# Kernel optimization log

Hardware: AMD Instinct MI355X
Metric: run time of the kernel (lower is better)

The kernel has to match this reference:

```python
import jax, jax.numpy as jnp
import numpy as np

ORDER = 63
CODEBOOK_SIZE = 256
MIN_DATA = 1
N_ITER = 5
EPS = 1e-05
PERTURB = 1e-05


def setup_inputs() -> dict:
    key = jax.random.key(0)
    x = jax.random.normal(key, (131072, ORDER + 1), dtype=jnp.float32)
    return {"x": x}


def _e_step(x, cb, T):
    # squared euclidean distances via gram trick: (T, curr)
    d2 = jnp.sum(x * x, 1)[:, None] - 2.0 * (x @ cb.T) + jnp.sum(cb * cb, 1)[None, :]
    idx = jnp.argmin(d2, axis=1)
    xq = cb[idx]
    dist = jnp.sum((x - xq) ** 2) / T
    return idx, dist


def _m_step(x, idx, curr, key):
    D = x.shape[1]
    ones = jnp.ones((x.shape[0],), x.dtype)
    n_data = jax.ops.segment_sum(ones, idx, num_segments=curr)        # histc
    mask = n_data >= MIN_DATA
    sums = jax.ops.segment_sum(x, idx, num_segments=curr)             # scatter_add
    cent = sums / jnp.maximum(n_data, 1.0)[:, None]
    m = jnp.argmax(n_data)
    r = jax.random.normal(key, (curr, D), x.dtype) * PERTURB
    nm = (~mask).astype(x.dtype)
    # empty clusters reseeded from the largest cluster, perturbed
    new = jnp.where(mask[:, None], cent, cent[m][None, :] - r)
    cnt = jnp.sum(nm)
    corr = jnp.sum(r * nm[:, None], axis=0) / jnp.maximum(cnt, 1.0)
    new = new.at[m].add(jnp.where(cnt > 0, corr, jnp.zeros_like(corr)))
    return new


def _lbg(x):
    T, D = x.shape
    K = CODEBOOK_SIZE
    codebook = jnp.full((K, D), 1e10, x.dtype).at[0].set(jnp.mean(x, axis=0))
    distance = jnp.asarray(jnp.inf, x.dtype)
    base = jax.random.key(42)
    curr = 1
    split = 0
    while curr * 2 <= K:  # static loop over log2(K) binary splits
        key_s = jax.random.fold_in(base, split)
        kr, kloop = jax.random.split(key_s)
        r = jax.random.normal(kr, (curr, D), x.dtype) * PERTURB
        codebook = codebook.at[curr:2 * curr].set(codebook[:curr] - r).at[:curr].add(r)
        curr *= 2
        prev = distance

        def body(carry, n, curr=curr):
            cb, prev_d, dist, done, key = carry
            idx, d_new = _e_step(x, cb, T)
            change = jnp.abs(prev_d - d_new)
            conv = (n > 0) & (change / (d_new + 1e-16) < EPS)
            key, sub = jax.random.split(key)
            cb_new = _m_step(x, idx, curr, sub)
            stop = done | conv
            cb_out = jnp.where(stop, cb, cb_new)        # skip m-step on convergence/break
            dist_out = jnp.where(done, dist, d_new)     # distance assigned before break
            prev_out = jnp.where(stop, prev_d, d_new)
            return (cb_out, prev_out, dist_out, stop, key), None

        carry0 = (codebook[:curr], prev, distance, jnp.asarray(False), kloop)
        (cb_fin, _, distance, _, _), _ = jax.lax.scan(body, carry0, jnp.arange(N_ITER))
        codebook = codebook.at[:curr].set(cb_fin)
        split += 1
    return codebook, distance


def reference(x):
    return _lbg(x)
```

## Files before the change

### kernel.cpp

```cpp
#include <hip/hip_runtime.h>
#include <stdint.h>


#define NPTS 131072
#define DIMS 64
#define KCB  256

struct LbgState { float dist; float prev; unsigned int done; unsigned int k0, k1; unsigned int pad; };

__device__ __forceinline__ uint32_t rotl32(uint32_t v, int n){ return (v<<n)|(v>>(32-n)); }

__device__ __forceinline__ void tf2x32(uint32_t k0, uint32_t k1, uint32_t x0, uint32_t x1,
                                       uint32_t& o0, uint32_t& o1){
  uint32_t ks2 = k0 ^ k1 ^ 0x1BD11BDAu;
  x0 += k0; x1 += k1;
  #define TFR(r) { x0 += x1; x1 = rotl32(x1, r); x1 ^= x0; }
  TFR(13) TFR(15) TFR(26) TFR(6)
  x0 += k1; x1 += ks2 + 1u;
  TFR(17) TFR(29) TFR(16) TFR(24)
  x0 += ks2; x1 += k0 + 2u;
  TFR(13) TFR(15) TFR(26) TFR(6)
  x0 += k0; x1 += k1 + 3u;
  TFR(17) TFR(29) TFR(16) TFR(24)
  x0 += k1; x1 += ks2 + 4u;
  TFR(13) TFR(15) TFR(26) TFR(6)
  x0 += ks2; x1 += k0 + 5u;
  #undef TFR
  o0 = x0; o1 = x1;
}

__device__ __forceinline__ float xla_erfinv_f32(float x){
  float w = -log1pf(-x*x);
  float p;
  if (w < 5.0f){
    w = w - 2.5f;
    p = 2.81022636e-08f;
    p = fmaf(p, w, 3.43273939e-07f);
    p = fmaf(p, w, -3.5233877e-06f);
    p = fmaf(p, w, -4.39150654e-06f);
    p = fmaf(p, w, 0.00021858087f);
    p = fmaf(p, w, -0.00125372503f);
    p = fmaf(p, w, -0.00417768164f);
    p = fmaf(p, w, 0.246640727f);
    p = fmaf(p, w, 1.50140941f);
  } else {
    w = sqrtf(w) - 3.0f;
    p = -0.000200214257f;
    p = fmaf(p, w, 0.000100950558f);
    p = fmaf(p, w, 0.00134934322f);
    p = fmaf(p, w, -0.00367342844f);
    p = fmaf(p, w, 0.00573950773f);
    p = fmaf(p, w, -0.0076224613f);
    p = fmaf(p, w, 0.00943887047f);
    p = fmaf(p, w, 1.00167406f);
    p = fmaf(p, w, 2.83297682f);
  }
  return p * x;
}

__device__ __forceinline__ float jax_normal_elem(uint32_t k0, uint32_t k1, uint32_t j){
  uint32_t o0, o1; tf2x32(k0, k1, 0u, j, o0, o1);
  uint32_t bits = o0 ^ o1;
  uint32_t fb = (bits >> 9) | 0x3f800000u;
  float f = __uint_as_float(fb) - 1.0f;
  const float lo = -0.99999994f;
  float u = f * 2.0f + lo;
  u = fmaxf(lo, u);
  return 1.41421356f * xla_erfinv_f32(u);
}

__device__ void do_split(float* __restrict__ cb, float* __restrict__ cnorm,
                         unsigned long long* __restrict__ sums,
                         unsigned int* __restrict__ ndata,
                         unsigned long long* __restrict__ distacc,
                         LbgState* __restrict__ st, int curr, int split, int t){
  __shared__ uint32_t kr0s, kr1s;
  if (t == 0){
    uint32_t ks0, ks1, a0, a1, b0, b1;
    tf2x32(0u, 42u, 0u, (uint32_t)split, ks0, ks1);
    tf2x32(ks0, ks1, 0u, 0u, a0, a1);
    tf2x32(ks0, ks1, 0u, 1u, b0, b1);
    kr0s = a0; kr1s = a1;
    st->k0 = b0; st->k1 = b1;
    st->prev = st->dist;
    st->done = 0u;
  }
  __syncthreads();
  const int n = curr * DIMS;
  for (int e = t; e < n; e += 256){
    int c = e >> 6, d = e & 63;
    float rv = jax_normal_elem(kr0s, kr1s, (uint32_t)e) * 1e-5f;
    float old = cb[c*DIMS + d];
    cb[(curr + c)*DIMS + d] = old - rv;
    cb[c*DIMS + d]          = old + rv;
  }
  __syncthreads();
  const int c2 = curr * 2;
  for (int c = t; c < c2; c += 256){
    float s = 0.f;
    for (int d = 0; d < DIMS; d++){ float vv = cb[c*DIMS+d]; s += vv*vv; }
    cnorm[c] = s;
  }
  for (int e = t; e < c2*DIMS; e += 256) sums[e] = 0ull;
  for (int c = t; c < c2; c += 256) ndata[c] = 0u;
  if (t == 0) *distacc = 0ull;
}

__global__ void mean_kernel(const float* __restrict__ x, unsigned long long* __restrict__ macc,
                            float* __restrict__ cb, float* __restrict__ cnorm,
                            unsigned long long* __restrict__ sums,
                            unsigned int* __restrict__ ndata,
                            unsigned long long* __restrict__ distacc,
                            LbgState* __restrict__ st, unsigned int* __restrict__ mcnt){
  __shared__ double part[256];
  __shared__ float stage[16*64];
  __shared__ int islast;
  const int t = threadIdx.x;
  const int d = t & 63;
  const int w = t >> 6;
  const size_t base = (size_t)blockIdx.x * 1024;
  const int lrow = t >> 4;
  const int lcol = (t & 15) * 4;

  const float4* xg = reinterpret_cast<const float4*>(x);
  float4 nxt = xg[((base + lrow) * DIMS + lcol) >> 2];
  double s = 0.0;
  for (int tt = 0; tt < 64; tt++){
    float4 cur = nxt;
    if (tt < 63)
      nxt = xg[((base + (tt+1)*16 + lrow) * DIMS + lcol) >> 2];
    __syncthreads();
    *reinterpret_cast<float4*>(&stage[lrow*DIMS + lcol]) = cur;
    __syncthreads();
    s += (double)stage[(w    )*DIMS + d];
    s += (double)stage[(w + 4)*DIMS + d];
    s += (double)stage[(w + 8)*DIMS + d];
    s += (double)stage[(w +12)*DIMS + d];
  }
  part[t] = s;
  __syncthreads();
  if (t < 64){
    double tot = part[t] + part[64+t] + part[128+t] + part[192+t];
    atomicAdd(&macc[t], (unsigned long long)__double2ll_rn(tot * 1099511627776.0));
  }
  __threadfence();
  __syncthreads();
  if (t == 0) islast = (atomicAdd(mcnt, 1u) == (unsigned)(gridDim.x - 1));
  __syncthreads();
  if (!islast) return;

  if (t < 64){
    long long mv = (long long)atomicAdd(&macc[t], 0ull);
    double mean = (double)mv * (1.0/1099511627776.0) / 131072.0;
    cb[t] = (float)mean;
  }
  for (int e = t; e < KCB*DIMS; e += 256)
    if (e >= 64) cb[e] = 1e10f;
  if (t == 0){
    st->dist = __builtin_inff();
    st->prev = __builtin_inff();
    st->done = 0u;
    atomicExch(mcnt, 0u);
  }
  __syncthreads();
  do_split(cb, cnorm, sums, ndata, distacc, st, 1, 0, t);
}

template<int CURR>
__global__ __launch_bounds__(256, 4)
void estep_kernel(const float* __restrict__ x, const float* __restrict__ cb,
                  const float* __restrict__ cnorm, unsigned char* __restrict__ bidx8,
                  unsigned long long* __restrict__ distacc, const LbgState* __restrict__ st){
  if (st->done) return;
  const int t = threadIdx.x;
  const int lane = t & 63;
  const int p = blockIdx.x * 256 + t;

  float xv[DIMS];
  const float4* xp = reinterpret_cast<const float4*>(x + (size_t)p * DIMS);
  #pragma unroll
  for (int i = 0; i < 16; i++){
    float4 v = xp[i];
    xv[4*i+0] = v.x; xv[4*i+1] = v.y; xv[4*i+2] = v.z; xv[4*i+3] = v.w;
  }
  float xx = 0.f;
  #pragma unroll
  for (int d = 0; d < DIMS; d++) xx += xv[d] * xv[d];

  constexpr int NJ = (CURR < 4) ? CURR : 4;
  float best = __builtin_inff();
  int bi = 0;
  for (int j0 = 0; j0 < CURR; j0 += NJ){
    const float* crow = cb + (size_t)j0 * DIMS;
    float acc[NJ];
    #pragma unroll
    for (int k = 0; k < NJ; k++) acc[k] = 0.f;
    #pragma unroll
    for (int d = 0; d < DIMS; d++){
      #pragma unroll
      for (int k = 0; k < NJ; k++)
        acc[k] = fmaf(xv[d], crow[k*DIMS + d], acc[k]);
    }
    #pragma unroll
    for (int k = 0; k < NJ; k++){
      float d2 = (xx - 2.0f*acc[k]) + cnorm[j0 + k];
      if (d2 < best){ best = d2; bi = j0 + k; }
    }
  }
  bidx8[p] = (unsigned char)bi;

  double dd = 0.0;
  const float4* cbv = reinterpret_cast<const float4*>(cb + (size_t)bi * DIMS);
  #pragma unroll
  for (int i = 0; i < 16; i++){
    float4 b = cbv[i];
    float df, sq;
    df = xv[4*i+0] - b.x; sq = df*df; dd += (double)sq;
    df = xv[4*i+1] - b.y; sq = df*df; dd += (double)sq;
    df = xv[4*i+2] - b.z; sq = df*df; dd += (double)sq;
    df = xv[4*i+3] - b.w; sq = df*df; dd += (double)sq;
  }
  for (int off = 32; off > 0; off >>= 1) dd += __shfl_down(dd, off);
  if (lane == 0)
    atomicAdd(distacc, (unsigned long long)__double2ll_rn(dd * 4294967296.0));
}

template<int CURR>
__global__ __launch_bounds__(256, 4)
void estep_sw(const float* __restrict__ x, const float* __restrict__ cb,
              const float* __restrict__ cnorm, unsigned char* __restrict__ bidx8,
              unsigned long long* __restrict__ distacc, const LbgState* __restrict__ st){
  if (st->done) return;
  constexpr int CPW = CURR / 4;
  constexpr int NJG = (CPW < 16) ? CPW : 16;
  constexpr int NG = CPW / NJG;
  __shared__ float4 xs[16*128];
  __shared__ float sxx[128];
  __shared__ float sbest[4*128];
  __shared__ int   sidx [4*128];
  __shared__ unsigned char sbidx[128];
  const int t = threadIdx.x;
  const int lane = t & 63;
  const int w = __builtin_amdgcn_readfirstlane(t >> 6);
  const int pbase = blockIdx.x * 128;

  {
    const int p = t & 127, h = t >> 7;
    const float4* xg = reinterpret_cast<const float4*>(x) + (size_t)(pbase + p) * 16 + h * 8;
    #pragma unroll
    for (int j = 0; j < 8; j++)
      xs[(h*8 + j)*128 + p] = xg[j];
  }
  __syncthreads();
  if (t < 128){
    float xx = 0.f;
    #pragma unroll
    for (int k4 = 0; k4 < 16; k4++){
      float4 v = xs[k4*128 + t];
      xx = fmaf(v.x, v.x, xx); xx = fmaf(v.y, v.y, xx);
      xx = fmaf(v.z, v.z, xx); xx = fmaf(v.w, v.w, xx);
    }
    sxx[t] = xx;
  }
  __syncthreads();

  const float xx0 = sxx[lane];
  const float xx1 = sxx[64 + lane];
  float best0 = __builtin_inff(), best1 = __builtin_inff();
  int bi0 = 0, bi1 = 0;
  const float4* cbg = reinterpret_cast<const float4*>(cb);
  const int cwbase = w * CPW;

  for (int g = 0; g < NG; g++){
    const int c0 = cwbase + g*NJG;
    float acc0[NJG], acc1[NJG];
    #pragma unroll
    for (int cj = 0; cj < NJG; cj++){ acc0[cj] = 0.f; acc1[cj] = 0.f; }
    for (int k4 = 0; k4 < 16; k4++){
      float4 xf0 = xs[k4*128 + lane];
      float4 xf1 = xs[k4*128 + 64 + lane];
      #pragma unroll
      for (int cj = 0; cj < NJG; cj++){
        float4 cf = cbg[(size_t)(c0 + cj)*16 + k4];
        acc0[cj] = fmaf(xf0.x, cf.x, acc0[cj]);
        acc0[cj] = fmaf(xf0.y, cf.y, acc0[cj]);
        acc0[cj] = fmaf(xf0.z, cf.z, acc0[cj]);
        acc0[cj] = fmaf(xf0.w, cf.w, acc0[cj]);
        acc1[cj] = fmaf(xf1.x, cf.x, acc1[cj]);
        acc1[cj] = fmaf(xf1.y, cf.y, acc1[cj]);
        acc1[cj] = fmaf(xf1.z, cf.z, acc1[cj]);
        acc1[cj] = fmaf(xf1.w, cf.w, acc1[cj]);
      }
    }
    #pragma unroll
    for (int cj = 0; cj < NJG; cj++){
      float cn = cnorm[c0 + cj];
      float d20 = (xx0 - 2.0f*acc0[cj]) + cn;
      if (d20 < best0){ best0 = d20; bi0 = c0 + cj; }
      float d21 = (xx1 - 2.0f*acc1[cj]) + cn;
      if (d21 < best1){ best1 = d21; bi1 = c0 + cj; }
    }
  }
  sbest[w*128 + lane]      = best0;  sidx[w*128 + lane]      = bi0;
  sbest[w*128 + 64 + lane] = best1;  sidx[w*128 + 64 + lane] = bi1;
  __syncthreads();

  if (t < 128){
    float best = sbest[t];
    int bi = sidx[t];
    #pragma unroll
    for (int ww = 1; ww < 4; ww++){
      float ob = sbest[ww*128 + t];
      int   oi = sidx [ww*128 + t];
      if (ob < best){ best = ob; bi = oi; }
    }
    sbidx[t] = (unsigned char)bi;
    bidx8[pbase + t] = (unsigned char)bi;
    const float4* cbv = cbg + (size_t)bi * 16;
    double dd = 0.0;
    #pragma unroll
    for (int k4 = 0; k4 < 16; k4++){
      float4 xv = xs[k4*128 + t];
      float4 b = cbv[k4];
      float df, sq;
      df = xv.x - b.x; sq = df*df; dd += (double)sq;
      df = xv.y - b.y; sq = df*df; dd += (double)sq;
      df = xv.z - b.z; sq = df*df; dd += (double)sq;
      df = xv.w - b.w; sq = df*df; dd += (double)sq;
    }
    for (int off = 32; off > 0; off >>= 1) dd += __shfl_down(dd, off);
    if ((t & 63) == 0)
      atomicAdd(distacc, (unsigned long long)__double2ll_rn(dd * 4294967296.0));
  }
}

template<int CURR, int NBLK>
__global__ __launch_bounds__(256)
void gather_kernel(const float* __restrict__ x, const unsigned char* __restrict__ bidx8,
                   unsigned long long* __restrict__ sums, unsigned int* __restrict__ ndata,
                   const LbgState* __restrict__ st){
  if (st->done) return;
  constexpr int CLOG = __builtin_ctz(CURR);
  constexpr int NCHUNK = NBLK / CURR;
  constexpr int PPC = NPTS / NCHUNK;
  constexpr int NPW = PPC / 4;
  __shared__ long long sacc[4*64];
  __shared__ unsigned int scw[4];
  const int t = threadIdx.x;
  const int lane = t & 63;
  const int w = t >> 6;
  const int c = blockIdx.x & (CURR - 1);
  const int chunk = blockIdx.x >> CLOG;
  const int pbase = chunk * PPC + w * NPW;

  long long acc = 0;
  unsigned int cnt = 0;
  int q0=0,q1=0,q2=0,q3=0,q4=0,q5=0,q6=0,q7=0, qn=0;
  const uint32_t* bp = reinterpret_cast<const uint32_t*>(bidx8 + pbase);
  for (int i = 0; i < NPW; i += 256){
    const uint32_t b4 = bp[(i >> 2) + lane];
    #pragma unroll
    for (int s = 0; s < 4; s++){
      unsigned long long m = __ballot(((b4 >> (8*s)) & 255u) == (unsigned)c);
      cnt += (unsigned int)__popcll(m);
      while (m){
        const int bit = __builtin_ctzll(m);
        m &= m - 1ull;
        const int p = pbase + i + bit*4 + s;
        if      (qn == 0) q0 = p;
        else if (qn == 1) q1 = p;
        else if (qn == 2) q2 = p;
        else if (qn == 3) q3 = p;
        else if (qn == 4) q4 = p;
        else if (qn == 5) q5 = p;
        else if (qn == 6) q6 = p;
        else              q7 = p;
        qn++;
        if (qn == 8){
          const float v0 = x[(size_t)q0 * DIMS + lane];
          const float v1 = x[(size_t)q1 * DIMS + lane];
          const float v2 = x[(size_t)q2 * DIMS + lane];
          const float v3 = x[(size_t)q3 * DIMS + lane];
          const float v4 = x[(size_t)q4 * DIMS + lane];
          const float v5 = x[(size_t)q5 * DIMS + lane];
          const float v6 = x[(size_t)q6 * DIMS + lane];
          const float v7 = x[(size_t)q7 * DIMS + lane];
          acc += (long long)__double2int_rn((double)v0 * 1048576.0);
          acc += (long long)__double2int_rn((double)v1 * 1048576.0);
          acc += (long long)__double2int_rn((double)v2 * 1048576.0);
          acc += (long long)__double2int_rn((double)v3 * 1048576.0);
          acc += (long long)__double2int_rn((double)v4 * 1048576.0);
          acc += (long long)__double2int_rn((double)v5 * 1048576.0);
          acc += (long long)__double2int_rn((double)v6 * 1048576.0);
          acc += (long long)__double2int_rn((double)v7 * 1048576.0);
          qn = 0;
        }
      }
    }
  }
  if (qn > 0){
    const int i1 = (qn > 1) ? q1 : q0;
    const int i2 = (qn > 2) ? q2 : q0;
    const int i3 = (qn > 3) ? q3 : q0;
    const int i4 = (qn > 4) ? q4 : q0;
    const int i5 = (qn > 5) ? q5 : q0;
    const int i6 = (qn > 6) ? q6 : q0;
    const float v0 = x[(size_t)q0 * DIMS + lane];
    const float v1 = x[(size_t)i1 * DIMS + lane];
    const float v2 = x[(size_t)i2 * DIMS + lane];
    const float v3 = x[(size_t)i3 * DIMS + lane];
    const float v4 = x[(size_t)i4 * DIMS + lane];
    const float v5 = x[(size_t)i5 * DIMS + lane];
    const float v6 = x[(size_t)i6 * DIMS + lane];
    acc += (long long)__double2int_rn((double)v0 * 1048576.0);
    if (qn > 1) acc += (long long)__double2int_rn((double)v1 * 1048576.0);
    if (qn > 2) acc += (long long)__double2int_rn((double)v2 * 1048576.0);
    if (qn > 3) acc += (long long)__double2int_rn((double)v3 * 1048576.0);
    if (qn > 4) acc += (long long)__double2int_rn((double)v4 * 1048576.0);
    if (qn > 5) acc += (long long)__double2int_rn((double)v5 * 1048576.0);
    if (qn > 6) acc += (long long)__double2int_rn((double)v6 * 1048576.0);
  }
  sacc[w*64 + lane] = acc;
  if (lane == 0) scw[w] = cnt;
  __syncthreads();
  if (w == 0){
    long long tot = sacc[lane] + sacc[64+lane] + sacc[128+lane] + sacc[192+lane];
    if (tot) atomicAdd(&sums[c*DIMS + lane], (unsigned long long)(tot * 1048576ll));
    if (lane == 0){
      unsigned int ct = scw[0] + scw[1] + scw[2] + scw[3];
      if (ct) atomicAdd(&ndata[c], ct);
    }
  }
}

__global__ void control_kernel(float* __restrict__ cb, float* __restrict__ cnorm,
                               unsigned long long* __restrict__ sums,
                               unsigned int* __restrict__ ndata,
                               unsigned long long* __restrict__ distacc,
                               LbgState* __restrict__ st, int curr, int n_iter,
                               int next_split){
  __shared__ int s_stop;
  __shared__ unsigned int sdone;
  __shared__ uint32_t sub0, sub1;
  __shared__ float cm[64];
  __shared__ int redv[256];
  __shared__ int redi[256];
  __shared__ int s_m, s_cnt;
  const int t = threadIdx.x;
  if (t == 0) sdone = st->done;
  __syncthreads();
  const unsigned int done0 = sdone;

  if (!done0){
    if (t == 0){
      double dd = (double)(long long)(*distacc) * (1.0/4294967296.0);
      float sf = (float)dd;
      float d_new = sf / 131072.0f;
      float change = fabsf(st->prev - d_new);
      int conv = (n_iter > 0) && (change / (d_new + 1e-16f) < 1e-5f);
      st->dist = d_new;
      if (!conv) st->prev = d_new;
      st->done = conv ? 1u : 0u;
      s_stop = conv;
      if (!conv){
        uint32_t a0, a1, b0, b1;
        tf2x32(st->k0, st->k1, 0u, 0u, a0, a1);
        tf2x32(st->k0, st->k1, 0u, 1u, b0, b1);
        st->k0 = a0; st->k1 = a1;
        sub0 = b0; sub1 = b1;
      }
    }
    __syncthreads();
    if (!s_stop){
      int v = (t < curr) ? (int)ndata[t] : -1;
      redv[t] = v; redi[t] = t;
      __syncthreads();
      for (int s = 128; s > 0; s >>= 1){
        if (t < s){
          if (redv[t+s] > redv[t] || (redv[t+s] == redv[t] && redi[t+s] < redi[t])){
            redv[t] = redv[t+s]; redi[t] = redi[t+s];
          }
        }
        __syncthreads();
      }
      if (t == 0) s_m = redi[0];
      __syncthreads();
      redv[t] = (t < curr && ndata[t] == 0u) ? 1 : 0;
      __syncthreads();
      for (int s = 128; s > 0; s >>= 1){
        if (t < s) redv[t] += redv[t+s];
        __syncthreads();
      }
      if (t == 0) s_cnt = redv[0];
      __syncthreads();
      const int m = s_m;
      const int cntE = s_cnt;

      if (t < 64){
        unsigned int nm_ = ndata[m]; if (nm_ < 1u) nm_ = 1u;
        double cd = (double)(long long)sums[m*DIMS + t] * (1.0/1099511627776.0) / (double)nm_;
        cm[t] = (float)cd;
      }
      __syncthreads();

      const int total = curr * DIMS;
      for (int e = t; e < total; e += 256){
        int c = e >> 6, d = e & 63;
        if (c == m) continue;
        float nv;
        unsigned int nd = ndata[c];
        if (nd >= 1u){
          double cd = (double)(long long)sums[e] * (1.0/1099511627776.0) / (double)nd;
          nv = (float)cd;
        } else {
          float rv = jax_normal_elem(sub0, sub1, (uint32_t)e) * 1e-5f;
          nv = cm[d] - rv;
        }
        cb[e] = nv;
      }
      if (t < 64){
        float add = 0.f;
        if (cntE > 0){
          float acc = 0.f;
          for (int c = 0; c < curr; c++){
            if (ndata[c] == 0u)
              acc += jax_normal_elem(sub0, sub1, (uint32_t)(c*DIMS + t)) * 1e-5f;
          }
          add = acc / fmaxf((float)cntE, 1.0f);
        }
        cb[m*DIMS + t] = cm[t] + add;
      }
      __syncthreads();

      for (int c = t; c < curr; c += 256){
        float s = 0.f;
        for (int d = 0; d < DIMS; d++){ float vv = cb[c*DIMS+d]; s += vv*vv; }
        cnorm[c] = s;
      }
      for (int e = t; e < total; e += 256) sums[e] = 0ull;
      for (int c = t; c < curr; c += 256) ndata[c] = 0u;
      if (t == 0) *distacc = 0ull;
    }
  }
  __syncthreads();
  if (n_iter == 4){
    if (curr < 256){
      do_split(cb, cnorm, sums, ndata, distacc, st, curr, next_split, t);
    } else if (t == 0){
      cb[KCB*DIMS] = st->dist;
    }
  }
}

extern "C" void kernel_launch(void* const* d_in, const int* in_sizes, int n_in,
                              void* d_out, int out_size, void* d_ws, size_t ws_size,
                              hipStream_t stream){
  const float* x = (const float*)d_in[0];
  float* cb = (float*)d_out;
  char* ws = (char*)d_ws;
  unsigned long long* sums    = (unsigned long long*)(ws + 0);
  unsigned long long* macc    = (unsigned long long*)(ws + 131072);
  unsigned long long* distacc = (unsigned long long*)(ws + 131584);
  LbgState* st                = (LbgState*)(ws + 131592);
  unsigned int* ndata         = (unsigned int*)(ws + 131616);
  float* cnorm                = (float*)(ws + 132640);
  unsigned char* bidx8        = (unsigned char*)(ws + 133664);
  unsigned int* mcnt          = (unsigned int*)(ws + 264736);

  hipMemsetAsync(d_ws, 0, 264744, stream);
  mean_kernel<<<128, 256, 0, stream>>>(x, macc, cb, cnorm, sums, ndata, distacc, st, mcnt);

  for (int split = 0; split < 8; split++){
    const int curr = 2 << split;
    for (int n = 0; n < 5; n++){
      switch (curr){
        case 2:   estep_kernel<2>  <<<512,256,0,stream>>>(x,cb,cnorm,bidx8,distacc,st);
                  gather_kernel<2,256>   <<<256, 256,0,stream>>>(x,bidx8,sums,ndata,st); break;
        case 4:   estep_kernel<4>  <<<512,256,0,stream>>>(x,cb,cnorm,bidx8,distacc,st);
                  gather_kernel<4,512>   <<<512, 256,0,stream>>>(x,bidx8,sums,ndata,st); break;
        case 8:   estep_sw<8>    <<<1024,256,0,stream>>>(x,cb,cnorm,bidx8,distacc,st);
                  gather_kernel<8,1024>  <<<1024,256,0,stream>>>(x,bidx8,sums,ndata,st); break;
        case 16:  estep_sw<16>   <<<1024,256,0,stream>>>(x,cb,cnorm,bidx8,distacc,st);
                  gather_kernel<16,2048> <<<2048,256,0,stream>>>(x,bidx8,sums,ndata,st); break;
        case 32:  estep_sw<32>   <<<1024,256,0,stream>>>(x,cb,cnorm,bidx8,distacc,st);
                  gather_kernel<32,2048> <<<2048,256,0,stream>>>(x,bidx8,sums,ndata,st); break;
        case 64:  estep_sw<64>   <<<1024,256,0,stream>>>(x,cb,cnorm,bidx8,distacc,st);
                  gather_kernel<64,2048> <<<2048,256,0,stream>>>(x,bidx8,sums,ndata,st); break;
        case 128: estep_sw<128>  <<<1024,256,0,stream>>>(x,cb,cnorm,bidx8,distacc,st);
                  gather_kernel<128,2048><<<2048,256,0,stream>>>(x,bidx8,sums,ndata,st); break;
        case 256: estep_sw<256>  <<<1024,256,0,stream>>>(x,cb,cnorm,bidx8,distacc,st);
                  gather_kernel<256,2048><<<2048,256,0,stream>>>(x,bidx8,sums,ndata,st); break;
      }
      control_kernel<<<1, 256, 0, stream>>>(cb, cnorm, sums, ndata, distacc, st, curr, n, split+1);
    }
  }
}
```

Measured before the change: 3.074 ms.

## Parallelize control kernel across blocks with ping-pong state buffers and vectorized gather

The single-block control kernel becomes a 16-block kernel. Each block updates a slice of codebook rows, and the split step is folded in. Accumulators and state are double-buffered so that blocks can read the previous iteration's inputs while zeroing the next set without a race. Gather loads switch from scalar per-lane loads to float4 loads over 4 rows per wave, with a transposed shared reduction. The tradeoffs are redundant argmax/count reductions in every block and more workspace.

```diff
diff --git a/kernel.cpp b/kernel.cpp
--- a/kernel.cpp
+++ b/kernel.cpp
@@ -5,6 +5,7 @@
 #define NPTS 131072
 #define DIMS 64
 #define KCB  256
+#define NCB  16
 
 struct LbgState { float dist; float prev; unsigned int done; unsigned int k0, k1; unsigned int pad; };
 
@@ -344,7 +345,7 @@
   constexpr int NCHUNK = NBLK / CURR;
   constexpr int PPC = NPTS / NCHUNK;
   constexpr int NPW = PPC / 4;
-  __shared__ long long sacc[4*64];
+  __shared__ long long sacc[4][64][4];
   __shared__ unsigned int scw[4];
   const int t = threadIdx.x;
   const int lane = t & 63;
@@ -352,8 +353,10 @@
   const int c = blockIdx.x & (CURR - 1);
   const int chunk = blockIdx.x >> CLOG;
   const int pbase = chunk * PPC + w * NPW;
-
-  long long acc = 0;
+  const int sub = lane >> 4;
+  const int dof = (lane & 15) * 4;
+
+  long long a0 = 0, a1 = 0, a2 = 0, a3 = 0;
   unsigned int cnt = 0;
   int q0=0,q1=0,q2=0,q3=0,q4=0,q5=0,q6=0,q7=0, qn=0;
   const uint32_t* bp = reinterpret_cast<const uint32_t*>(bidx8 + pbase);
@@ -377,22 +380,18 @@
         else              q7 = p;
         qn++;
         if (qn == 8){
-          const float v0 = x[(size_t)q0 * DIMS + lane];
-          const float v1 = x[(size_t)q1 * DIMS + lane];
-          const float v2 = x[(size_t)q2 * DIMS + lane];
-          const float v3 = x[(size_t)q3 * DIMS + lane];
-          const float v4 = x[(size_t)q4 * DIMS + lane];
-          const float v5 = x[(size_t)q5 * DIMS + lane];
-          const float v6 = x[(size_t)q6 * DIMS + lane];
-          const float v7 = x[(size_t)q7 * DIMS + lane];
-          acc += (long long)__double2int_rn((double)v0 * 1048576.0);
-          acc += (long long)__double2int_rn((double)v1 * 1048576.0);
-          acc += (long long)__double2int_rn((double)v2 * 1048576.0);
-          acc += (long long)__double2int_rn((double)v3 * 1048576.0);
-          acc += (long long)__double2int_rn((double)v4 * 1048576.0);
-          acc += (long long)__double2int_rn((double)v5 * 1048576.0);
-          acc += (long long)__double2int_rn((double)v6 * 1048576.0);
-          acc += (long long)__double2int_rn((double)v7 * 1048576.0);
+          const int rA = (sub==0)?q0:(sub==1)?q1:(sub==2)?q2:q3;
+          const int rB = (sub==0)?q4:(sub==1)?q5:(sub==2)?q6:q7;
+          const float4 vA = *reinterpret_cast<const float4*>(x + (size_t)rA * DIMS + dof);
+          const float4 vB = *reinterpret_cast<const float4*>(x + (size_t)rB * DIMS + dof);
+          a0 += (long long)__double2int_rn((double)vA.x * 1048576.0);
+          a1 += (long long)__double2int_rn((double)vA.y * 1048576.0);
+          a2 += (long long)__double2int_rn((double)vA.z * 1048576.0);
+          a3 += (long long)__double2int_rn((double)vA.w * 1048576.0);
+          a0 += (long long)__double2int_rn((double)vB.x * 1048576.0);
+          a1 += (long long)__double2int_rn((double)vB.y * 1048576.0);
+          a2 += (long long)__double2int_rn((double)vB.z * 1048576.0);
+          a3 += (long long)__double2int_rn((double)vB.w * 1048576.0);
           qn = 0;
         }
       }
@@ -405,26 +404,34 @@
     const int i4 = (qn > 4) ? q4 : q0;
     const int i5 = (qn > 5) ? q5 : q0;
     const int i6 = (qn > 6) ? q6 : q0;
-    const float v0 = x[(size_t)q0 * DIMS + lane];
-    const float v1 = x[(size_t)i1 * DIMS + lane];
-    const float v2 = x[(size_t)i2 * DIMS + lane];
-    const float v3 = x[(size_t)i3 * DIMS + lane];
-    const float v4 = x[(size_t)i4 * DIMS + lane];
-    const float v5 = x[(size_t)i5 * DIMS + lane];
-    const float v6 = x[(size_t)i6 * DIMS + lane];
-    acc += (long long)__double2int_rn((double)v0 * 1048576.0);
-    if (qn > 1) acc += (long long)__double2int_rn((double)v1 * 1048576.0);
-    if (qn > 2) acc += (long long)__double2int_rn((double)v2 * 1048576.0);
-    if (qn > 3) acc += (long long)__double2int_rn((double)v3 * 1048576.0);
-    if (qn > 4) acc += (long long)__double2int_rn((double)v4 * 1048576.0);
-    if (qn > 5) acc += (long long)__double2int_rn((double)v5 * 1048576.0);
-    if (qn > 6) acc += (long long)__double2int_rn((double)v6 * 1048576.0);
-  }
-  sacc[w*64 + lane] = acc;
+    const int rA = (sub==0)?q0:(sub==1)?i1:(sub==2)?i2:i3;
+    const int rB = (sub==0)?i4:(sub==1)?i5:(sub==2)?i6:q0;
+    const float4 vA = *reinterpret_cast<const float4*>(x + (size_t)rA * DIMS + dof);
+    const float4 vB = *reinterpret_cast<const float4*>(x + (size_t)rB * DIMS + dof);
+    if (sub < qn){
+      a0 += (long long)__double2int_rn((double)vA.x * 1048576.0);
+      a1 += (long long)__double2int_rn((double)vA.y * 1048576.0);
+      a2 += (long long)__double2int_rn((double)vA.z * 1048576.0);
+      a3 += (long long)__double2int_rn((double)vA.w * 1048576.0);
+    }
+    if (sub + 4 < qn){
+      a0 += (long long)__double2int_rn((double)vB.x * 1048576.0);
+      a1 += (long long)__double2int_rn((double)vB.y * 1048576.0);
+      a2 += (long long)__double2int_rn((double)vB.z * 1048576.0);
+      a3 += (long long)__double2int_rn((double)vB.w * 1048576.0);
+    }
+  }
+  sacc[w][lane][0] = a0; sacc[w][lane][1] = a1;
+  sacc[w][lane][2] = a2; sacc[w][lane][3] = a3;
   if (lane == 0) scw[w] = cnt;
   __syncthreads();
   if (w == 0){
-    long long tot = sacc[lane] + sacc[64+lane] + sacc[128+lane] + sacc[192+lane];
+    long long tot = 0;
+    #pragma unroll
+    for (int ww = 0; ww < 4; ww++)
+      #pragma unroll
+      for (int r = 0; r < 4; r++)
+        tot += sacc[ww][r*16 + (lane >> 2)][lane & 3];
     if (tot) atomicAdd(&sums[c*DIMS + lane], (unsigned long long)(tot * 1048576ll));
     if (lane == 0){
       unsigned int ct = scw[0] + scw[1] + scw[2] + scw[3];
@@ -434,120 +441,163 @@
 }
 
 __global__ void control_kernel(float* __restrict__ cb, float* __restrict__ cnorm,
-                               unsigned long long* __restrict__ sums,
-                               unsigned int* __restrict__ ndata,
-                               unsigned long long* __restrict__ distacc,
-                               LbgState* __restrict__ st, int curr, int n_iter,
-                               int next_split){
-  __shared__ int s_stop;
-  __shared__ unsigned int sdone;
-  __shared__ uint32_t sub0, sub1;
+                               const unsigned long long* __restrict__ sums_in,
+                               unsigned long long* __restrict__ sums_out,
+                               const unsigned int* __restrict__ ndata_in,
+                               unsigned int* __restrict__ ndata_out,
+                               const unsigned long long* __restrict__ distacc_in,
+                               unsigned long long* __restrict__ distacc_out,
+                               const LbgState* __restrict__ st_in,
+                               LbgState* __restrict__ st_out,
+                               int curr, int n_iter, int next_split){
   __shared__ float cm[64];
   __shared__ int redv[256];
   __shared__ int redi[256];
   __shared__ int s_m, s_cnt;
   const int t = threadIdx.x;
-  if (t == 0) sdone = st->done;
-  __syncthreads();
-  const unsigned int done0 = sdone;
-
+  const int b = blockIdx.x;
+
+  const unsigned int done0 = st_in->done;
+  float d_new = 0.f;
+  int stop = 1;
+  uint32_t sub0 = 0, sub1 = 0, nk0 = 0, nk1 = 0;
   if (!done0){
-    if (t == 0){
-      double dd = (double)(long long)(*distacc) * (1.0/4294967296.0);
-      float sf = (float)dd;
-      float d_new = sf / 131072.0f;
-      float change = fabsf(st->prev - d_new);
-      int conv = (n_iter > 0) && (change / (d_new + 1e-16f) < 1e-5f);
-      st->dist = d_new;
-      if (!conv) st->prev = d_new;
-      st->done = conv ? 1u : 0u;
-      s_stop = conv;
-      if (!conv){
-        uint32_t a0, a1, b0, b1;
-        tf2x32(st->k0, st->k1, 0u, 0u, a0, a1);
-        tf2x32(st->k0, st->k1, 0u, 1u, b0, b1);
-        st->k0 = a0; st->k1 = a1;
-        sub0 = b0; sub1 = b1;
-      }
-    }
-    __syncthreads();
-    if (!s_stop){
-      int v = (t < curr) ? (int)ndata[t] : -1;
-      redv[t] = v; redi[t] = t;
+    double ddv = (double)(long long)(*distacc_in) * (1.0/4294967296.0);
+    float sf = (float)ddv;
+    d_new = sf / 131072.0f;
+    float change = fabsf(st_in->prev - d_new);
+    int conv = (n_iter > 0) && (change / (d_new + 1e-16f) < 1e-5f);
+    stop = conv;
+    if (!conv){
+      tf2x32(st_in->k0, st_in->k1, 0u, 0u, nk0, nk1);
+      tf2x32(st_in->k0, st_in->k1, 0u, 1u, sub0, sub1);
+    }
+  }
+
+  const int rpb = (curr + NCB - 1) / NCB;
+  const int r0 = b * rpb;
+  int r1 = r0 + rpb; if (r1 > curr) r1 = curr;
+
+  if (!done0 && !stop){
+    int v = (t < curr) ? (int)ndata_in[t] : -1;
+    redv[t] = v; redi[t] = t;
+    __syncthreads();
+    for (int s = 128; s > 0; s >>= 1){
+      if (t < s){
+        if (redv[t+s] > redv[t] || (redv[t+s] == redv[t] && redi[t+s] < redi[t])){
+          redv[t] = redv[t+s]; redi[t] = redi[t+s];
+        }
+      }
       __syncthreads();
-      for (int s = 128; s > 0; s >>= 1){
-        if (t < s){
-          if (redv[t+s] > redv[t] || (redv[t+s] == redv[t] && redi[t+s] < redi[t])){
-            redv[t] = redv[t+s]; redi[t] = redi[t+s];
-          }
+    }
+    if (t == 0) s_m = redi[0];
+    __syncthreads();
+    redv[t] = (t < curr && ndata_in[t] == 0u) ? 1 : 0;
+    __syncthreads();
+    for (int s = 128; s > 0; s >>= 1){
+      if (t < s) redv[t] += redv[t+s];
+      __syncthreads();
+    }
+    if (t == 0) s_cnt = redv[0];
+    __syncthreads();
+    const int m = s_m;
+    const int cntE = s_cnt;
+
+    if (t < 64){
+      unsigned int nm_ = ndata_in[m]; if (nm_ < 1u) nm_ = 1u;
+      double cd = (double)(long long)sums_in[m*DIMS + t] * (1.0/1099511627776.0) / (double)nm_;
+      cm[t] = (float)cd;
+    }
+    __syncthreads();
+
+    for (int e = r0*DIMS + t; e < r1*DIMS; e += 256){
+      int cc = e >> 6, d = e & 63;
+      if (cc == m) continue;
+      float nv;
+      unsigned int nd = ndata_in[cc];
+      if (nd >= 1u){
+        double cd = (double)(long long)sums_in[e] * (1.0/1099511627776.0) / (double)nd;
+        nv = (float)cd;
+      } else {
+        float rv = jax_normal_elem(sub0, sub1, (uint32_t)e) * 1e-5f;
+        nv = cm[d] - rv;
+      }
+      cb[e] = nv;
+    }
+    if (m >= r0 && m < r1 && t < 64){
+      float add = 0.f;
+      if (cntE > 0){
+        float acc = 0.f;
+        for (int cc = 0; cc < curr; cc++){
+          if (ndata_in[cc] == 0u)
+            acc += jax_normal_elem(sub0, sub1, (uint32_t)(cc*DIMS + t)) * 1e-5f;
         }
-        __syncthreads();
-      }
-      if (t == 0) s_m = redi[0];
-      __syncthreads();
-      redv[t] = (t < curr && ndata[t] == 0u) ? 1 : 0;
-      __syncthreads();
-      for (int s = 128; s > 0; s >>= 1){
-        if (t < s) redv[t] += redv[t+s];
-        __syncthreads();
-      }
-      if (t == 0) s_cnt = redv[0];
-      __syncthreads();
-      const int m = s_m;
-      const int cntE = s_cnt;
-
-      if (t < 64){
-        unsigned int nm_ = ndata[m]; if (nm_ < 1u) nm_ = 1u;
-        double cd = (double)(long long)sums[m*DIMS + t] * (1.0/1099511627776.0) / (double)nm_;
-        cm[t] = (float)cd;
-      }
-      __syncthreads();
-
-      const int total = curr * DIMS;
-      for (int e = t; e < total; e += 256){
-        int c = e >> 6, d = e & 63;
-        if (c == m) continue;
-        float nv;
-        unsigned int nd = ndata[c];
-        if (nd >= 1u){
-          double cd = (double)(long long)sums[e] * (1.0/1099511627776.0) / (double)nd;
-          nv = (float)cd;
-        } else {
-          float rv = jax_normal_elem(sub0, sub1, (uint32_t)e) * 1e-5f;
-          nv = cm[d] - rv;
-        }
-        cb[e] = nv;
-      }
-      if (t < 64){
-        float add = 0.f;
-        if (cntE > 0){
-          float acc = 0.f;
-          for (int c = 0; c < curr; c++){
-            if (ndata[c] == 0u)
-              acc += jax_normal_elem(sub0, sub1, (uint32_t)(c*DIMS + t)) * 1e-5f;
-          }
-          add = acc / fmaxf((float)cntE, 1.0f);
-        }
-        cb[m*DIMS + t] = cm[t] + add;
-      }
-      __syncthreads();
-
-      for (int c = t; c < curr; c += 256){
-        float s = 0.f;
-        for (int d = 0; d < DIMS; d++){ float vv = cb[c*DIMS+d]; s += vv*vv; }
-        cnorm[c] = s;
-      }
-      for (int e = t; e < total; e += 256) sums[e] = 0ull;
-      for (int c = t; c < curr; c += 256) ndata[c] = 0u;
-      if (t == 0) *distacc = 0ull;
-    }
-  }
-  __syncthreads();
-  if (n_iter == 4){
-    if (curr < 256){
-      do_split(cb, cnorm, sums, ndata, distacc, st, curr, next_split, t);
-    } else if (t == 0){
-      cb[KCB*DIMS] = st->dist;
+        add = acc / fmaxf((float)cntE, 1.0f);
+      }
+      cb[m*DIMS + t] = cm[t] + add;
+    }
+    __syncthreads();
+
+    for (int cc = r0 + t; cc < r1; cc += 256){
+      float s = 0.f;
+      for (int d = 0; d < DIMS; d++){ float vv = cb[cc*DIMS+d]; s += vv*vv; }
+      cnorm[cc] = s;
+    }
+  }
+
+  const int rows_next = (n_iter == 4 && curr < KCB) ? 2*curr : curr;
+  for (int e = b*256 + t; e < rows_next*DIMS; e += NCB*256) sums_out[e] = 0ull;
+  for (int cc = b*256 + t; cc < rows_next; cc += NCB*256) ndata_out[cc] = 0u;
+  if (b == 0 && t == 0) *distacc_out = 0ull;
+
+  if (b == 0 && t == 0){
+    const float fin_dist = done0 ? st_in->dist : d_new;
+    LbgState ns;
+    ns.dist = fin_dist;
+    if (done0 || stop){
+      ns.prev = st_in->prev; ns.done = 1u; ns.k0 = st_in->k0; ns.k1 = st_in->k1;
+    } else {
+      ns.prev = d_new; ns.done = 0u; ns.k0 = nk0; ns.k1 = nk1;
+    }
+    ns.pad = 0u;
+    if (n_iter == 4){
+      if (curr < KCB){
+        uint32_t ks0, ks1, sa0, sa1, sb0, sb1;
+        tf2x32(0u, 42u, 0u, (uint32_t)next_split, ks0, ks1);
+        tf2x32(ks0, ks1, 0u, 0u, sa0, sa1);
+        tf2x32(ks0, ks1, 0u, 1u, sb0, sb1);
+        ns.k0 = sb0; ns.k1 = sb1;
+        ns.prev = fin_dist;
+        ns.done = 0u;
+      } else {
+        cb[KCB*DIMS] = fin_dist;
+      }
+    }
+    *st_out = ns;
+  }
+
+  if (n_iter == 4 && curr < KCB){
+    uint32_t ks0, ks1, kr0, kr1, t0, t1;
+    tf2x32(0u, 42u, 0u, (uint32_t)next_split, ks0, ks1);
+    tf2x32(ks0, ks1, 0u, 0u, kr0, kr1);
+    (void)t0; (void)t1;
+    __syncthreads();
+    for (int e = r0*DIMS + t; e < r1*DIMS; e += 256){
+      int cc = e >> 6, d = e & 63;
+      float rv = jax_normal_elem(kr0, kr1, (uint32_t)e) * 1e-5f;
+      float old = cb[e];
+      cb[(curr + cc)*DIMS + d] = old - rv;
+      cb[e]                    = old + rv;
+    }
+    __syncthreads();
+    for (int cc = r0 + t; cc < r1; cc += 256){
+      float s0 = 0.f, s1 = 0.f;
+      for (int d = 0; d < DIMS; d++){
+        float v0 = cb[cc*DIMS + d];        s0 += v0*v0;
+        float v1 = cb[(curr+cc)*DIMS + d]; s1 += v1*v1;
+      }
+      cnorm[cc] = s0;
+      cnorm[curr + cc] = s1;
     }
   }
 }
@@ -558,40 +608,54 @@
   const float* x = (const float*)d_in[0];
   float* cb = (float*)d_out;
   char* ws = (char*)d_ws;
-  unsigned long long* sums    = (unsigned long long*)(ws + 0);
-  unsigned long long* macc    = (unsigned long long*)(ws + 131072);
-  unsigned long long* distacc = (unsigned long long*)(ws + 131584);
-  LbgState* st                = (LbgState*)(ws + 131592);
-  unsigned int* ndata         = (unsigned int*)(ws + 131616);
-  float* cnorm                = (float*)(ws + 132640);
-  unsigned char* bidx8        = (unsigned char*)(ws + 133664);
-  unsigned int* mcnt          = (unsigned int*)(ws + 264736);
-
-  hipMemsetAsync(d_ws, 0, 264744, stream);
-  mean_kernel<<<128, 256, 0, stream>>>(x, macc, cb, cnorm, sums, ndata, distacc, st, mcnt);
-
+  unsigned long long* sums0   = (unsigned long long*)(ws + 0);
+  unsigned long long* sums1   = (unsigned long long*)(ws + 131072);
+  unsigned long long* macc    = (unsigned long long*)(ws + 262144);
+  unsigned long long* dist0   = (unsigned long long*)(ws + 262656);
+  unsigned long long* dist1   = (unsigned long long*)(ws + 262664);
+  LbgState* st0               = (LbgState*)(ws + 262672);
+  LbgState* st1               = (LbgState*)(ws + 262704);
+  unsigned int* nd0           = (unsigned int*)(ws + 262736);
+  unsigned int* nd1           = (unsigned int*)(ws + 263760);
+  float* cnorm                = (float*)(ws + 264784);
+  unsigned char* bidx8        = (unsigned char*)(ws + 265808);
+  unsigned int* mcnt          = (unsigned int*)(ws + 396880);
+
+  unsigned long long* sums[2] = { sums0, sums1 };
+  unsigned long long* dac[2]  = { dist0, dist1 };
+  LbgState* st[2]             = { st0, st1 };
+  unsigned int* nd[2]         = { nd0, nd1 };
+
+  hipMemsetAsync(d_ws, 0, 396884, stream);
+  mean_kernel<<<128, 256, 0, stream>>>(x, macc, cb, cnorm, sums0, nd0, dist0, st0, mcnt);
+
+  int g = 0;
   for (int split = 0; split < 8; split++){
     const int curr = 2 << split;
     for (int n = 0; n < 5; n++){
+      const int pi = g & 1, po = pi ^ 1;
       switch (curr){
-        case 2:   estep_kernel<2>  <<<512,256,0,stream>>>(x,cb,cnorm,bidx8,distacc,st);
-                  gather_kernel<2,256>   <<<256, 256,0,stream>>>(x,bidx8,sums,ndata,st); break;
-        case 4:   estep_kernel<4>  <<<512,256,0,stream>>>(x,cb,cnorm,bidx8,distacc,st);
-                  gather_kernel<4,512>   <<<512, 256,0,stream>>>(x,bidx8,sums,ndata,st); break;
-        case 8:   estep_sw<8>    <<<1024,256,0,stream>>>(x,cb,cnorm,bidx8,distacc,st);
-                  gather_kernel<8,1024>  <<<1024,256,0,stream>>>(x,bidx8,sums,ndata,st); break;
-        case 16:  estep_sw<16>   <<<1024,256,0,stream>>>(x,cb,cnorm,bidx8,distacc,st);
-                  gather_kernel<16,2048> <<<2048,256,0,stream>>>(x,bidx8,sums,ndata,st); break;
-        case 32:  estep_sw<32>   <<<1024,256,0,stream>>>(x,cb,cnorm,bidx8,distacc,st);
-                  gather_kernel<32,2048> <<<2048,256,0,stream>>>(x,bidx8,sums,ndata,st); break;
-        case 64:  estep_sw<64>   <<<1024,256,0,stream>>>(x,cb,cnorm,bidx8,distacc,st);
-                  gather_kernel<64,2048> <<<2048,256,0,stream>>>(x,bidx8,sums,ndata,st); break;
-        case 128: estep_sw<128>  <<<1024,256,0,stream>>>(x,cb,cnorm,bidx8,distacc,st);
-                  gather_kernel<128,2048><<<2048,256,0,stream>>>(x,bidx8,sums,ndata,st); break;
-        case 256: estep_sw<256>  <<<1024,256,0,stream>>>(x,cb,cnorm,bidx8,distacc,st);
-                  gather_kernel<256,2048><<<2048,256,0,stream>>>(x,bidx8,sums,ndata,st); break;
-      }
-      control_kernel<<<1, 256, 0, stream>>>(cb, cnorm, sums, ndata, distacc, st, curr, n, split+1);
-    }
-  }
-}
+        case 2:   estep_kernel<2>  <<<512,256,0,stream>>>(x,cb,cnorm,bidx8,dac[pi],st[pi]);
+                  gather_kernel<2,256>   <<<256, 256,0,stream>>>(x,bidx8,sums[pi],nd[pi],st[pi]); break;
+        case 4:   estep_kernel<4>  <<<512,256,0,stream>>>(x,cb,cnorm,bidx8,dac[pi],st[pi]);
+                  gather_kernel<4,512>   <<<512, 256,0,stream>>>(x,bidx8,sums[pi],nd[pi],st[pi]); break;
+        case 8:   estep_sw<8>    <<<1024,256,0,stream>>>(x,cb,cnorm,bidx8,dac[pi],st[pi]);
+                  gather_kernel<8,1024>  <<<1024,256,0,stream>>>(x,bidx8,sums[pi],nd[pi],st[pi]); break;
+        case 16:  estep_sw<16>   <<<1024,256,0,stream>>>(x,cb,cnorm,bidx8,dac[pi],st[pi]);
+                  gather_kernel<16,2048> <<<2048,256,0,stream>>>(x,bidx8,sums[pi],nd[pi],st[pi]); break;
+        case 32:  estep_sw<32>   <<<1024,256,0,stream>>>(x,cb,cnorm,bidx8,dac[pi],st[pi]);
+                  gather_kernel<32,2048> <<<2048,256,0,stream>>>(x,bidx8,sums[pi],nd[pi],st[pi]); break;
+        case 64:  estep_sw<64>   <<<1024,256,0,stream>>>(x,cb,cnorm,bidx8,dac[pi],st[pi]);
+                  gather_kernel<64,2048> <<<2048,256,0,stream>>>(x,bidx8,sums[pi],nd[pi],st[pi]); break;
+        case 128: estep_sw<128>  <<<1024,256,0,stream>>>(x,cb,cnorm,bidx8,dac[pi],st[pi]);
+                  gather_kernel<128,2048><<<2048,256,0,stream>>>(x,bidx8,sums[pi],nd[pi],st[pi]); break;
+        case 256: estep_sw<256>  <<<1024,256,0,stream>>>(x,cb,cnorm,bidx8,dac[pi],st[pi]);
+                  gather_kernel<256,2048><<<2048,256,0,stream>>>(x,bidx8,sums[pi],nd[pi],st[pi]); break;
+      }
+      control_kernel<<<NCB, 256, 0, stream>>>(cb, cnorm,
+          sums[pi], sums[po], nd[pi], nd[po], dac[pi], dac[po],
+          st[pi], st[po], curr, n, split+1);
+      g++;
+    }
+  }
+}
```

After: 2.721 ms. -11.5%, faster.
